# Kernel tuning notes

Hardware: AMD Instinct MI355X
Metric: run time of the kernel (lower is better)

## Reference

```python
import jax, jax.numpy as jnp
import numpy as np

B, S, E, H = 4, 2048, 1024, 16
D = E // H  # head_size = 64


def setup_inputs() -> dict:
    key = jax.random.key(0)
    k1, k2 = jax.random.split(key)
    x = jax.random.normal(k1, (B, S, E), dtype=jnp.float32)
    # fused QKV projection weight (torch Linear(E, 3E, bias=False))
    W_qkv = jax.random.normal(k2, (E, 3 * E), dtype=jnp.float32) * (1.0 / np.sqrt(E))
    return {"x": x, "W_qkv": W_qkv}


def reference(x, W_qkv):
    b, s, e = x.shape
    qkv = x @ W_qkv                              # [B,S,3E]
    q, k, v = jnp.split(qkv, 3, axis=-1)
    # [B,S,E] -> [B,H,S,D]
    q = q.reshape(b, s, H, D).transpose(0, 2, 1, 3)
    k = k.reshape(b, s, H, D).transpose(0, 2, 1, 3)
    v = v.reshape(b, s, H, D).transpose(0, 2, 1, 3)
    scores = jnp.einsum("bhqd,bhkd->bhqk", q, k) * (1.0 / np.sqrt(D))
    causal = jnp.tril(jnp.ones((s, s), dtype=bool))  # [S,S]
    scores = jnp.where(causal[None, None, :, :], scores, jnp.float32(-jnp.inf))
    attn = jax.nn.softmax(scores, axis=-1)
    # dropout is identity in eval mode (p effectively 0 for this baseline)
    out = jnp.einsum("bhqk,bhkd->bhqd", attn, v)  # [B,H,S,D]
    out = out.transpose(0, 2, 1, 3).reshape(b, s, e)
    # NOTE: original forward never applies output_projection; faithful omission.
    return out
```

## Files before the change

### kernel.cpp

```cpp
#include <hip/hip_runtime.h>
#include <hip/hip_bf16.h>
#include <cstdint>
#include <cstddef>

#define GLOBAL_AS __attribute__((address_space(1)))
#define LDS_AS __attribute__((address_space(3)))

typedef short bf16x8 __attribute__((ext_vector_type(8)));
typedef float f32x4 __attribute__((ext_vector_type(4)));

constexpr int Bq = 4, Sq = 2048, Eq = 1024, Hh = 16;
constexpr int M = Bq * Sq;
constexpr int K = 1024;
constexpr int N = 3 * Eq;

#define SMSC 0.18033688f
#define SMBIAS (-16.0f)

#if __has_builtin(__builtin_amdgcn_exp2f)
#define EXP2F(x) __builtin_amdgcn_exp2f(x)
#else
#define EXP2F(x) exp2f(x)
#endif

static __device__ __forceinline__ unsigned f2bf(float f) {
    union { float f; unsigned u; } v; v.f = f;
    unsigned r = v.u + 0x7fffu + ((v.u >> 16) & 1u);
    return r >> 16;
}

static __device__ __forceinline__ unsigned pk2(float a, float b) {
    union { __hip_bfloat162 h; unsigned u; } c;
    c.h = __float22bfloat162_rn(float2{a, b});
    return c.u;
}

__global__ __launch_bounds__(256) void prep(const float* __restrict__ X,
                                            unsigned short* __restrict__ Xb,
                                            const float* __restrict__ W,
                                            unsigned short* __restrict__ Wt) {
    __shared__ unsigned short tile[64 * 72];
    const int t = threadIdx.x;
    const int bx = blockIdx.x;
    if (bx < 4096) {
        size_t i = ((size_t)bx * 256 + t) * 8;
        float4 a = *reinterpret_cast<const float4*>(X + i);
        float4 b = *reinterpret_cast<const float4*>(X + i + 4);
        uint4 o;
        o.x = pk2(a.x, a.y);
        o.y = pk2(a.z, a.w);
        o.z = pk2(b.x, b.y);
        o.w = pk2(b.z, b.w);
        *reinterpret_cast<uint4*>(Xb + i) = o;
        return;
    }
    const int idx = bx - 4096;
    const int n0 = (idx % 48) * 64;
    const int k0 = (idx / 48) * 64;
    #pragma unroll
    for (int p = 0; p < 4; ++p) {
        int c = p * 256 + t;
        int row = c >> 4;
        int c4 = (c & 15) * 4;
        float4 v = *reinterpret_cast<const float4*>(W + (size_t)(k0 + row) * N + n0 + c4);
        *reinterpret_cast<unsigned*>(&tile[row * 72 + c4]) = pk2(v.x, v.y);
        *reinterpret_cast<unsigned*>(&tile[row * 72 + c4 + 2]) = pk2(v.z, v.w);
    }
    __syncthreads();
    #pragma unroll
    for (int p = 0; p < 2; ++p) {
        int c = t + p * 256;
        int n = c & 63;
        int kc = (c >> 6) * 8;
        unsigned v[8];
        #pragma unroll
        for (int j = 0; j < 8; ++j) v[j] = tile[(kc + j) * 72 + n];
        uint4 o;
        o.x = v[0] | (v[1] << 16);
        o.y = v[2] | (v[3] << 16);
        o.z = v[4] | (v[5] << 16);
        o.w = v[6] | (v[7] << 16);
        *reinterpret_cast<uint4*>(Wt + (size_t)(n0 + n) * K + k0 + kc) = o;
    }
}

__global__ __launch_bounds__(256) void gemm_qkv(const unsigned short* __restrict__ A,
                                                const unsigned short* __restrict__ Bt,
                                                unsigned short* __restrict__ C,
                                                unsigned short* __restrict__ Vt) {
    __shared__ unsigned short Alds[128 * 64];
    __shared__ unsigned short Blds[128 * 64];
    const int t = threadIdx.x;
    const int lane = t & 63, w = t >> 6;
    const int wm = w >> 1, wn = w & 1;
    const int m0 = blockIdx.y * 128, n0 = blockIdx.x * 128;
    const int lr = lane & 15, quad = lane >> 4;
    const int sw = lr & 7;

    f32x4 acc[4][4] = {};
    for (int k0 = 0; k0 < K; k0 += 64) {
        #pragma unroll
        for (int p = 0; p < 4; ++p) {
            int c = p * 256 + t;
            int row = c >> 3;
            int lch = (c & 7) ^ (row & 7);
            const unsigned short* ga = A + (size_t)(m0 + row) * K + k0 + lch * 8;
            __builtin_amdgcn_global_load_lds((const GLOBAL_AS unsigned int*)ga,
                                             (LDS_AS unsigned int*)&Alds[c * 8], 16, 0, 0);
            const unsigned short* gb = Bt + (size_t)(n0 + row) * K + k0 + lch * 8;
            __builtin_amdgcn_global_load_lds((const GLOBAL_AS unsigned int*)gb,
                                             (LDS_AS unsigned int*)&Blds[c * 8], 16, 0, 0);
        }
        __syncthreads();
        #pragma unroll
        for (int ks = 0; ks < 2; ++ks) {
            bf16x8 af[4], bfr[4];
            const int pch = ((ks * 4 + quad) ^ sw) << 3;
            #pragma unroll
            for (int mt = 0; mt < 4; ++mt)
                af[mt] = *reinterpret_cast<const bf16x8*>(
                    &Alds[(wm * 64 + mt * 16 + lr) * 64 + pch]);
            #pragma unroll
            for (int nt = 0; nt < 4; ++nt)
                bfr[nt] = *reinterpret_cast<const bf16x8*>(
                    &Blds[(wn * 64 + nt * 16 + lr) * 64 + pch]);
            #pragma unroll
            for (int mt = 0; mt < 4; ++mt)
                #pragma unroll
                for (int nt = 0; nt < 4; ++nt)
                    acc[mt][nt] = __builtin_amdgcn_mfma_f32_16x16x32_bf16(af[mt], bfr[nt],
                                                                          acc[mt][nt], 0, 0, 0);
        }
        __syncthreads();
    }
    if (n0 < 2 * Eq) {
        #pragma unroll
        for (int mt = 0; mt < 4; ++mt)
            #pragma unroll
            for (int nt = 0; nt < 4; ++nt)
                #pragma unroll
                for (int r = 0; r < 4; ++r) {
                    int row = m0 + wm * 64 + mt * 16 + quad * 4 + r;
                    int col = n0 + wn * 64 + nt * 16 + lr;
                    C[(size_t)row * N + col] = (unsigned short)f2bf(acc[mt][nt][r]);
                }
    } else {
        const int b2 = m0 >> 11;
        const int sbase = (m0 & 2047) + wm * 64;
        #pragma unroll
        for (int mt = 0; mt < 4; ++mt)
            #pragma unroll
            for (int nt = 0; nt < 4; ++nt) {
                int hd = n0 - 2 * Eq + wn * 64 + nt * 16 + lr;
                size_t rowV = (size_t)(b2 * Hh + (hd >> 6)) * 64 + (hd & 63);
                int s = sbase + mt * 16 + quad * 4;
                uint2 val;
                val.x = f2bf(acc[mt][nt][0]) | (f2bf(acc[mt][nt][1]) << 16);
                val.y = f2bf(acc[mt][nt][2]) | (f2bf(acc[mt][nt][3]) << 16);
                *reinterpret_cast<uint2*>(Vt + rowV * Sq + s) = val;
            }
    }
}

__global__ __launch_bounds__(256, 4) void flash_attn(const unsigned short* __restrict__ QKV,
                                                     const unsigned short* __restrict__ Vt,
                                                     float* __restrict__ Out) {
    __shared__ unsigned short Klds[2][32 * 64];
    __shared__ unsigned short Vlds[2][64 * 32];
    __shared__ unsigned short Plds[4][32 * 40];
    const int t = threadIdx.x;
    const int lane = t & 63, w = t >> 6;
    const int lr = lane & 15, quad = lane >> 4;
    const int hb = blockIdx.x;
    const int h = hb & 15, b = hb >> 4;
    const int i = 15 - (int)blockIdx.y;
    const int jmax = 4 * i + 3;
    const int jd = 4 * i + w;
    const int qbase = i * 128 + w * 32;
    unsigned short* Pl = Plds[w];
    const int sw = lr & 7;

    const unsigned short* Kbase = QKV + (size_t)b * Sq * N + Eq + h * 64;
    const unsigned short* Vbase = Vt + (size_t)((b * Hh + h) * 64) * Sq;

    bf16x8 ones;
    #pragma unroll
    for (int z = 0; z < 8; ++z) ones[z] = (short)0x3F80;

    auto stage = [&](int j, int buf) {
        const int kv0 = j * 32;
        {
            int row = t >> 3;
            int lch = (t & 7) ^ (row & 7);
            const unsigned short* gk = Kbase + (size_t)(kv0 + row) * N + lch * 8;
            __builtin_amdgcn_global_load_lds((const GLOBAL_AS unsigned int*)gk,
                                             (LDS_AS unsigned int*)&Klds[buf][t * 8], 16, 0, 0);
        }
        {
            int row = t >> 2;
            int ch = t & 3;
            const unsigned short* gv = Vbase + (size_t)row * Sq + kv0 + ch * 8;
            __builtin_amdgcn_global_load_lds((const GLOBAL_AS unsigned int*)gv,
                                             (LDS_AS unsigned int*)&Vlds[buf][t * 8], 16, 0, 0);
        }
    };

    bf16x8 qf[2][2];
    #pragma unroll
    for (int mt = 0; mt < 2; ++mt)
        #pragma unroll
        for (int ks = 0; ks < 2; ++ks)
            qf[mt][ks] = *reinterpret_cast<const bf16x8*>(
                QKV + (size_t)(b * Sq + qbase + mt * 16 + lr) * N + h * 64 + ks * 32 + quad * 8);

    f32x4 o[2][4] = {};
    f32x4 lsum[2] = {};

    stage(0, 0);
    int cur = 0;
    for (int j = 0; j <= jmax; ++j) {
        __syncthreads();
        if (j < jmax) stage(j + 1, cur ^ 1);

        if (j <= jd) {
            const unsigned short* Kb = Klds[cur];
            const unsigned short* Vb = Vlds[cur];
            const int kv0 = j * 32;

            f32x4 sa[2][2] = {};
            #pragma unroll
            for (int ks = 0; ks < 2; ++ks) {
                const int pch = ((ks * 4 + quad) ^ sw) << 3;
                #pragma unroll
                for (int nt = 0; nt < 2; ++nt) {
                    bf16x8 kf = *reinterpret_cast<const bf16x8*>(&Kb[(nt * 16 + lr) * 64 + pch]);
                    #pragma unroll
                    for (int mt = 0; mt < 2; ++mt)
                        sa[mt][nt] = __builtin_amdgcn_mfma_f32_16x16x32_bf16(qf[mt][ks], kf,
                                                                             sa[mt][nt], 0, 0, 0);
                }
            }

            if (j == jd) {
                #pragma unroll
                for (int mt = 0; mt < 2; ++mt)
                    #pragma unroll
                    for (int nt = 0; nt < 2; ++nt)
                        #pragma unroll
                        for (int r = 0; r < 4; ++r) {
                            int qg = qbase + mt * 16 + quad * 4 + r;
                            int kvg = kv0 + nt * 16 + lr;
                            float sc = fmaf(sa[mt][nt][r], SMSC, SMBIAS);
                            sc = (kvg > qg) ? -1e30f : sc;
                            Pl[(mt * 16 + quad * 4 + r) * 40 + nt * 16 + lr] =
                                (unsigned short)(__float_as_uint(EXP2F(sc)) >> 16);
                        }
            } else {
                #pragma unroll
                for (int mt = 0; mt < 2; ++mt)
                    #pragma unroll
                    for (int nt = 0; nt < 2; ++nt)
                        #pragma unroll
                        for (int r = 0; r < 4; ++r)
                            Pl[(mt * 16 + quad * 4 + r) * 40 + nt * 16 + lr] =
                                (unsigned short)(__float_as_uint(
                                    EXP2F(fmaf(sa[mt][nt][r], SMSC, SMBIAS))) >> 16);
            }
            asm volatile("s_waitcnt lgkmcnt(0)" ::: "memory");

            bf16x8 pf[2];
            #pragma unroll
            for (int mt = 0; mt < 2; ++mt)
                pf[mt] = *reinterpret_cast<const bf16x8*>(&Pl[(mt * 16 + lr) * 40 + quad * 8]);

            #pragma unroll
            for (int dt = 0; dt < 4; ++dt) {
                bf16x8 vf = *reinterpret_cast<const bf16x8*>(&Vb[(dt * 16 + lr) * 32 + quad * 8]);
                #pragma unroll
                for (int mt = 0; mt < 2; ++mt)
                    o[mt][dt] = __builtin_amdgcn_mfma_f32_16x16x32_bf16(pf[mt], vf,
                                                                        o[mt][dt], 0, 0, 0);
            }
            #pragma unroll
            for (int mt = 0; mt < 2; ++mt)
                lsum[mt] = __builtin_amdgcn_mfma_f32_16x16x32_bf16(pf[mt], ones,
                                                                   lsum[mt], 0, 0, 0);
        }
        cur ^= 1;
    }

    #pragma unroll
    for (int mt = 0; mt < 2; ++mt)
        #pragma unroll
        for (int r = 0; r < 4; ++r) {
            float inv = 1.0f / lsum[mt][r];
            int qg = qbase + mt * 16 + quad * 4 + r;
            #pragma unroll
            for (int dt = 0; dt < 4; ++dt)
                Out[(size_t)(b * Sq + qg) * Eq + h * 64 + dt * 16 + lr] = o[mt][dt][r] * inv;
        }
}

extern "C" void kernel_launch(void* const* d_in, const int* in_sizes, int n_in,
                              void* d_out, int out_size, void* d_ws, size_t ws_size,
                              hipStream_t stream) {
    const float* x  = (const float*)d_in[0];
    const float* Wq = (const float*)d_in[1];
    float* out = (float*)d_out;

    unsigned short* xb  = (unsigned short*)d_ws;
    unsigned short* qkv = xb + (size_t)M * K;
    unsigned short* Wt  = qkv + (size_t)M * N;
    unsigned short* Vt  = Wt + (size_t)N * K;

    prep<<<dim3(4096 + 768), 256, 0, stream>>>(x, xb, Wq, Wt);
    gemm_qkv<<<dim3(N / 128, M / 128), 256, 0, stream>>>(xb, Wt, qkv, Vt);
    flash_attn<<<dim3(Hh * Bq, 16), 256, 0, stream>>>(qkv, Vt, out);
}
```

Measured before the change: 213.5 us.

## Keep softmax probabilities in registers via transposed QK^T and permlane swaps

Computes S^T by swapping the MFMA operand order, so each lane holds scores along the key dimension. The probabilities are then packed to bf16 and rearranged across lanes with v_permlane32/16_swap into the A-operand layout for the PV MFMA. This removes the per-wave LDS round trip for P (store, lgkmcnt wait, reload) and the Plds buffer. In exchange it adds cross-lane permute instructions, and it relies on the permuted layout matching the MFMA operand layout exactly. Rounding also changes from truncation to round-to-nearest.

After: 214.4 us. No clear change (+0.4%).

```diff
diff --git a/kernel.cpp b/kernel.cpp
--- a/kernel.cpp
+++ b/kernel.cpp
@@ -33,6 +33,13 @@
     union { __hip_bfloat162 h; unsigned u; } c;
     c.h = __float22bfloat162_rn(float2{a, b});
     return c.u;
+}
+
+static __device__ __forceinline__ void pl32swap(unsigned& a, unsigned& b) {
+    asm("v_permlane32_swap_b32 %0, %1" : "+v"(a), "+v"(b));
+}
+static __device__ __forceinline__ void pl16swap(unsigned& a, unsigned& b) {
+    asm("v_permlane16_swap_b32 %0, %1" : "+v"(a), "+v"(b));
 }
 
 __global__ __launch_bounds__(256) void prep(const float* __restrict__ X,
@@ -167,7 +174,6 @@
                                                      float* __restrict__ Out) {
     __shared__ unsigned short Klds[2][32 * 64];
     __shared__ unsigned short Vlds[2][64 * 32];
-    __shared__ unsigned short Plds[4][32 * 40];
     const int t = threadIdx.x;
     const int lane = t & 63, w = t >> 6;
     const int lr = lane & 15, quad = lane >> 4;
@@ -177,7 +183,6 @@
     const int jmax = 4 * i + 3;
     const int jd = 4 * i + w;
     const int qbase = i * 128 + w * 32;
-    unsigned short* Pl = Plds[w];
     const int sw = lr & 7;
 
     const unsigned short* Kbase = QKV + (size_t)b * Sq * N + Eq + h * 64;
@@ -232,59 +237,65 @@
             for (int ks = 0; ks < 2; ++ks) {
                 const int pch = ((ks * 4 + quad) ^ sw) << 3;
                 #pragma unroll
-                for (int nt = 0; nt < 2; ++nt) {
-                    bf16x8 kf = *reinterpret_cast<const bf16x8*>(&Kb[(nt * 16 + lr) * 64 + pch]);
+                for (int kt = 0; kt < 2; ++kt) {
+                    bf16x8 kf = *reinterpret_cast<const bf16x8*>(&Kb[(kt * 16 + lr) * 64 + pch]);
                     #pragma unroll
-                    for (int mt = 0; mt < 2; ++mt)
-                        sa[mt][nt] = __builtin_amdgcn_mfma_f32_16x16x32_bf16(qf[mt][ks], kf,
-                                                                             sa[mt][nt], 0, 0, 0);
+                    for (int qt = 0; qt < 2; ++qt)
+                        sa[kt][qt] = __builtin_amdgcn_mfma_f32_16x16x32_bf16(kf, qf[qt][ks],
+                                                                             sa[kt][qt], 0, 0, 0);
                 }
             }
 
+            float p[2][2][4];
             if (j == jd) {
                 #pragma unroll
-                for (int mt = 0; mt < 2; ++mt)
+                for (int kt = 0; kt < 2; ++kt)
                     #pragma unroll
-                    for (int nt = 0; nt < 2; ++nt)
+                    for (int qt = 0; qt < 2; ++qt)
                         #pragma unroll
                         for (int r = 0; r < 4; ++r) {
-                            int qg = qbase + mt * 16 + quad * 4 + r;
-                            int kvg = kv0 + nt * 16 + lr;
-                            float sc = fmaf(sa[mt][nt][r], SMSC, SMBIAS);
+                            int kvg = kv0 + kt * 16 + quad * 4 + r;
+                            int qg = qbase + qt * 16 + lr;
+                            float sc = fmaf(sa[kt][qt][r], SMSC, SMBIAS);
                             sc = (kvg > qg) ? -1e30f : sc;
-                            Pl[(mt * 16 + quad * 4 + r) * 40 + nt * 16 + lr] =
-                                (unsigned short)(__float_as_uint(EXP2F(sc)) >> 16);
+                            p[kt][qt][r] = EXP2F(sc);
                         }
             } else {
                 #pragma unroll
-                for (int mt = 0; mt < 2; ++mt)
+                for (int kt = 0; kt < 2; ++kt)
                     #pragma unroll
-                    for (int nt = 0; nt < 2; ++nt)
+                    for (int qt = 0; qt < 2; ++qt)
                         #pragma unroll
                         for (int r = 0; r < 4; ++r)
-                            Pl[(mt * 16 + quad * 4 + r) * 40 + nt * 16 + lr] =
-                                (unsigned short)(__float_as_uint(
-                                    EXP2F(fmaf(sa[mt][nt][r], SMSC, SMBIAS))) >> 16);
-            }
-            asm volatile("s_waitcnt lgkmcnt(0)" ::: "memory");
-
-            bf16x8 pf[2];
-            #pragma unroll
-            for (int mt = 0; mt < 2; ++mt)
-                pf[mt] = *reinterpret_cast<const bf16x8*>(&Pl[(mt * 16 + lr) * 40 + quad * 8]);
+                            p[kt][qt][r] = EXP2F(fmaf(sa[kt][qt][r], SMSC, SMBIAS));
+            }
+
+            bf16x8 af[2];
+            #pragma unroll
+            for (int qt = 0; qt < 2; ++qt) {
+                unsigned w00 = pk2(p[0][qt][0], p[0][qt][1]);
+                unsigned w01 = pk2(p[0][qt][2], p[0][qt][3]);
+                unsigned w10 = pk2(p[1][qt][0], p[1][qt][1]);
+                unsigned w11 = pk2(p[1][qt][2], p[1][qt][3]);
+                pl32swap(w00, w10); pl16swap(w00, w10);
+                pl32swap(w01, w11); pl16swap(w01, w11);
+                union { unsigned u[4]; bf16x8 v; } pa;
+                pa.u[0] = w00; pa.u[1] = w01; pa.u[2] = w10; pa.u[3] = w11;
+                af[qt] = pa.v;
+            }
 
             #pragma unroll
             for (int dt = 0; dt < 4; ++dt) {
                 bf16x8 vf = *reinterpret_cast<const bf16x8*>(&Vb[(dt * 16 + lr) * 32 + quad * 8]);
                 #pragma unroll
-                for (int mt = 0; mt < 2; ++mt)
-                    o[mt][dt] = __builtin_amdgcn_mfma_f32_16x16x32_bf16(pf[mt], vf,
-                                                                        o[mt][dt], 0, 0, 0);
-            }
-            #pragma unroll
-            for (int mt = 0; mt < 2; ++mt)
-                lsum[mt] = __builtin_amdgcn_mfma_f32_16x16x32_bf16(pf[mt], ones,
-                                                                   lsum[mt], 0, 0, 0);
+                for (int qt = 0; qt < 2; ++qt)
+                    o[qt][dt] = __builtin_amdgcn_mfma_f32_16x16x32_bf16(af[qt], vf,
+                                                                        o[qt][dt], 0, 0, 0);
+            }
+            #pragma unroll
+            for (int qt = 0; qt < 2; ++qt)
+                lsum[qt] = __builtin_amdgcn_mfma_f32_16x16x32_bf16(af[qt], ones,
+                                                                   lsum[qt], 0, 0, 0);
         }
         cur ^= 1;
     }
```
